# Kernel tuning notes

Hardware: AMD Instinct MI355X
Metric: run time of the kernel (lower is better)

The kernel has to match this reference:

```python
import jax, jax.numpy as jnp
import numpy as np
import math

D_MODEL = 1024
N_HEADS = 16
HEAD_DIM = D_MODEL // N_HEADS
PAD_INDEX = 0
NEG_INF = -1e9  # matches torch masked_fill value


def setup_inputs() -> dict:
    key = jax.random.key(0)
    ks = jax.random.split(key, 10)
    b, s = 2, 2048
    x = jax.random.normal(ks[0], (b, s, D_MODEL), dtype=jnp.float32)
    input_ids = jax.random.randint(ks[1], (b, s), 0, 32000, dtype=jnp.int64)
    scale = 1.0 / math.sqrt(D_MODEL)
    def lin(k):
        kw, kb = jax.random.split(k)
        W = jax.random.uniform(kw, (D_MODEL, D_MODEL), jnp.float32, -scale, scale)
        bb = jax.random.uniform(kb, (D_MODEL,), jnp.float32, -scale, scale)
        return W, bb
    Wq, bq = lin(ks[2])
    Wk, bk = lin(ks[3])
    Wv, bv = lin(ks[4])
    Wo, bo = lin(ks[5])
    return {"x": x, "input_ids": input_ids,
            "Wq": Wq, "bq": bq, "Wk": Wk, "bk": bk,
            "Wv": Wv, "bv": bv, "Wo": Wo, "bo": bo}


def reference(x, input_ids, Wq, bq, Wk, bk, Wv, bv, Wo, bo):
    b, s, _ = x.shape
    # torch nn.Linear: y = x @ W.T + b
    q = (x @ Wq.T + bq).reshape(b, s, N_HEADS, HEAD_DIM)
    k = (x @ Wk.T + bk).reshape(b, s, N_HEADS, HEAD_DIM)
    v = (x @ Wv.T + bv).reshape(b, s, N_HEADS, HEAD_DIM)
    # scores: [b, h, s, s]
    scores = jnp.einsum('bqhd,bkhd->bhqk', q, k) / math.sqrt(HEAD_DIM)
    pad_mask = (input_ids != PAD_INDEX)[:, None, None, :]          # [b,1,1,s] over keys
    causal = jnp.tril(jnp.ones((s, s), dtype=bool))[None, None]     # [1,1,s,s]
    final_mask = pad_mask & causal
    scores = jnp.where(final_mask, scores, NEG_INF)
    attn = jax.nn.softmax(scores, axis=-1)
    out = jnp.einsum('bhqk,bkhd->bqhd', attn, v).reshape(b, s, D_MODEL)
    return out @ Wo.T + bo
```

## Files before the change

### kernel.cpp

```cpp
#include <hip/hip_runtime.h>

#define DMODEL 1024
#define NHEADS 16
#define HDIM   64
#define BATCH  2
#define SEQ    2048
#define MROWS  (BATCH*SEQ)

typedef __bf16 bf16x8 __attribute__((ext_vector_type(8)));
typedef __bf16 bf16x4 __attribute__((ext_vector_type(4)));
typedef float floatx4 __attribute__((ext_vector_type(4)));

typedef const __attribute__((address_space(1))) void gvoid;
typedef __attribute__((address_space(3))) void lvoid;

template<bool V> struct ICb { static constexpr bool value = V; };

#define QSCALE 0.18033688011112042f

__global__ void cast_all(const float* __restrict__ x,
                         const float* __restrict__ wq, const float* __restrict__ wk,
                         const float* __restrict__ wv, const float* __restrict__ wo,
                         __bf16* __restrict__ xb, __bf16* __restrict__ wqb,
                         __bf16* __restrict__ wkb, __bf16* __restrict__ wvb,
                         __bf16* __restrict__ wob)
{
  const int i = blockIdx.x * 256 + threadIdx.x;
  const float* s; __bf16* o; int off;
  if (i < MROWS*DMODEL/4) { s = x; o = xb; off = i; }
  else {
    const int r = i - MROWS*DMODEL/4;
    const int w = r >> 18;
    off = r & 262143;
    s = (w == 0) ? wq : (w == 1) ? wk : (w == 2) ? wv : wo;
    o = (w == 0) ? wqb : (w == 1) ? wkb : (w == 2) ? wvb : wob;
  }
  const float4 f = ((const float4*)s)[off];
  bf16x4 v = {(__bf16)f.x, (__bf16)f.y, (__bf16)f.z, (__bf16)f.w};
  *(bf16x4*)(o + off*4) = v;
}

template<int MODE>
__global__ __launch_bounds__(256, 3)
void gemm_nt(const unsigned short* __restrict__ A,
             const unsigned short* __restrict__ W0,
             const unsigned short* __restrict__ W1,
             const unsigned short* __restrict__ W2,
             const float* __restrict__ b0,
             const float* __restrict__ b1,
             const float* __restrict__ b2,
             unsigned short* __restrict__ qout,
             unsigned short* __restrict__ kout,
             unsigned short* __restrict__ vout,
             float* __restrict__ outf)
{
  const int K = DMODEL;
  __shared__ unsigned short As[2][128*32];
  __shared__ unsigned short Bs[2][128*32];
  const int tid  = threadIdx.x;
  const int wid  = tid >> 6;
  const int lane = tid & 63;

  const int lin = blockIdx.x;
  const int wg  = (MODE == 0) ? ((lin & 7)*96 + (lin >> 3))
                              : ((lin & 7)*32 + (lin >> 3));
  const int bx  = (MODE == 0) ? (wg % 24) : (wg & 7);
  const int by  = (MODE == 0) ? (wg / 24) : (wg >> 3);
  const int brow = by * 128;
  const int bcol = bx * 128;
  const int wr = (wid >> 1) * 64;
  const int wc = (wid & 1) * 64;

  int which = 0;
  const unsigned short* Bw = W0;
  const float* bias = b0;
  int bcolL = bcol;
  if (MODE == 0) {
    which = bcol >> 10;
    Bw   = which == 0 ? W0 : which == 1 ? W1 : W2;
    bias = which == 0 ? b0 : which == 1 ? b1 : b2;
    bcolL = bcol & 1023;
  }

  floatx4 acc[4][4] = {};

  const int sr = wid*16 + (lane >> 2);
  const int sc = (lane & 3) * 8;
  const int fr = lane & 15;
  const int fk = (lane >> 4) * 8;

#define GSTAGE(KT, B) do {                                                     \
    _Pragma("unroll")                                                          \
    for (int i_ = 0; i_ < 2; ++i_) {                                           \
      __builtin_amdgcn_global_load_lds(                                        \
          (gvoid*)(A + (size_t)(brow + i_*64 + sr)*K + (KT) + sc),             \
          (lvoid*)(As[B] + i_*2048 + wid*512), 16, 0, 0);                      \
      __builtin_amdgcn_global_load_lds(                                        \
          (gvoid*)(Bw + (size_t)(bcolL + i_*64 + sr)*K + (KT) + sc),           \
          (lvoid*)(Bs[B] + i_*2048 + wid*512), 16, 0, 0);                      \
    }                                                                          \
  } while (0)

  GSTAGE(0, 0);

  for (int kt = 0; kt < K; kt += 32) {
    const int cur = (kt >> 5) & 1;
    if (kt + 32 < K) {
      GSTAGE(kt + 32, cur ^ 1);
      asm volatile("s_waitcnt vmcnt(4)" ::: "memory");
    } else {
      asm volatile("s_waitcnt vmcnt(0)" ::: "memory");
    }
    __builtin_amdgcn_s_barrier();
    __builtin_amdgcn_sched_barrier(0);

    bf16x8 af[4], bfv[4];
#pragma unroll
    for (int m = 0; m < 4; ++m)
      af[m] = *(const bf16x8*)(As[cur] + (wr + m*16 + fr)*32 + fk);
#pragma unroll
    for (int n = 0; n < 4; ++n)
      bfv[n] = *(const bf16x8*)(Bs[cur] + (wc + n*16 + fr)*32 + fk);
    __builtin_amdgcn_s_setprio(1);
#pragma unroll
    for (int m = 0; m < 4; ++m)
#pragma unroll
      for (int n = 0; n < 4; ++n)
        acc[m][n] = __builtin_amdgcn_mfma_f32_16x16x32_bf16(af[m], bfv[n], acc[m][n], 0, 0, 0);
    __builtin_amdgcn_s_setprio(0);
    __builtin_amdgcn_s_barrier();
  }
#undef GSTAGE

  const int er = (lane >> 4) * 4;
  const int ec = lane & 15;
#pragma unroll
  for (int m = 0; m < 4; ++m) {
#pragma unroll
    for (int n = 0; n < 4; ++n) {
      const int colL = bcolL + wc + n*16 + ec;
      const float bv = bias[colL];
      const int rowb = brow + wr + m*16 + er;
      if (MODE == 0) {
        const int bi = rowb >> 11, s = rowb & 2047;
        const int hh = colL >> 6, dd = colL & 63;
        if (which == 2) {
          bf16x4 v4 = {(__bf16)(acc[m][n][0] + bv), (__bf16)(acc[m][n][1] + bv),
                       (__bf16)(acc[m][n][2] + bv), (__bf16)(acc[m][n][3] + bv)};
          *(bf16x4*)((__bf16*)vout + ((size_t)(bi*NHEADS + hh)*HDIM + dd)*SEQ + s) = v4;
        } else if (which == 0) {
          __bf16* o = (__bf16*)qout;
#pragma unroll
          for (int j = 0; j < 4; ++j)
            o[((size_t)(bi*NHEADS + hh)*SEQ + s + j)*HDIM + dd] =
                (__bf16)((acc[m][n][j] + bv) * QSCALE);
        } else {
          __bf16* o = (__bf16*)kout;
#pragma unroll
          for (int j = 0; j < 4; ++j)
            o[((size_t)(bi*NHEADS + hh)*SEQ + s + j)*HDIM + dd] = (__bf16)(acc[m][n][j] + bv);
        }
      } else {
#pragma unroll
        for (int j = 0; j < 4; ++j)
          outf[(size_t)(rowb + j)*DMODEL + colL] = acc[m][n][j] + bv;
      }
    }
  }
}

__global__ __launch_bounds__(128, 4)
void attn_fwd(const unsigned short* __restrict__ qb,
              const unsigned short* __restrict__ kb,
              const unsigned short* __restrict__ vtb,
              const int* __restrict__ ids,
              unsigned short* __restrict__ outb)
{
  const int lin = blockIdx.x;
  const int k8 = lin >> 8;
  const int c8 = lin & 255;
  const int hb = c8 & 31;
  const int j  = c8 >> 5;
  const int qt = k8*8 + ((k8 & 1) ? 7 - j : j);
  const int h = hb & 15, bi = hb >> 4;

  const int tid = threadIdx.x, wid = tid >> 6, lane = tid & 63;
  const size_t hoff = (size_t)(bi*NHEADS + h) * SEQ * HDIM;
  const unsigned short* Qh  = qb  + hoff;
  const unsigned short* Kh  = kb  + hoff;
  const unsigned short* Vth = vtb + hoff;

  __shared__ unsigned short Ks[2][32*64];
  __shared__ unsigned short Vs[2][64*32];
  __shared__ unsigned short Ps[2][16*32];

  const int q_   = lane & 15;
  const int hi4  = lane >> 4;
  const int koff = hi4 * 4;
  const int qg = qt*32 + wid*16 + q_;

  bf16x8 qf[2];
#pragma unroll
  for (int c = 0; c < 2; ++c)
    qf[c] = *(const bf16x8*)(Qh + (size_t)qg*HDIM + c*32 + hi4*8);

  const int kr0 = tid >> 3;
  const int kc  = ((tid & 7) ^ (kr0 & 7)) * 8;
  const int vd0 = tid >> 2;
  const int vc  = ((tid & 3) ^ (vd0 & 3)) * 8;
  unsigned short* Pw = Ps[wid];

#define STAGE(T, B) do {                                                       \
    const unsigned short* kb_ = Kh + (size_t)(T)*32*HDIM;                      \
    const unsigned short* vb_ = Vth + (T)*32;                                  \
    __builtin_amdgcn_global_load_lds((gvoid*)(kb_ + kr0*HDIM + kc),            \
                                     (lvoid*)(Ks[B] + tid*8), 16, 0, 0);       \
    __builtin_amdgcn_global_load_lds((gvoid*)(kb_ + (kr0+16)*HDIM + kc),       \
                                     (lvoid*)(Ks[B] + (tid+128)*8), 16, 0, 0); \
    __builtin_amdgcn_global_load_lds((gvoid*)(vb_ + (size_t)vd0*SEQ + vc),     \
                                     (lvoid*)(Vs[B] + tid*8), 16, 0, 0);       \
    __builtin_amdgcn_global_load_lds((gvoid*)(vb_ + (size_t)(vd0+32)*SEQ + vc),\
                                     (lvoid*)(Vs[B] + (tid+128)*8), 16, 0, 0); \
  } while (0)

  float lsum = 0.f;
  floatx4 Oacc[4] = {};

  auto step = [&](auto Mc, int kb0, int bufc, unsigned int wm) {
    constexpr bool MASKED = decltype(Mc)::value;

    floatx4 st[2];
    __builtin_amdgcn_s_setprio(1);
#pragma unroll
    for (int t = 0; t < 2; ++t) {
      st[t] = (floatx4){0.f, 0.f, 0.f, 0.f};
      const int kr = t*16 + q_;
#pragma unroll
      for (int c = 0; c < 2; ++c) {
        bf16x8 kf = *(const bf16x8*)(Ks[bufc] + kr*64 + (((c*4 + hi4) ^ (q_ & 7)) * 8));
        st[t] = __builtin_amdgcn_mfma_f32_16x16x32_bf16(kf, qf[c], st[t], 0, 0, 0);
      }
    }
    __builtin_amdgcn_s_setprio(0);

    float ps = 0.f;
#pragma unroll
    for (int t = 0; t < 2; ++t) {
      float p[4];
#pragma unroll
      for (int r = 0; r < 4; ++r) {
        float pv = exp2f(st[t][r]);
        if (MASKED) {
          const int ko = t*16 + koff + r;
          const bool dead = ((kb0 + ko) > qg) || (((wm >> ko) & 1u) != 0u);
          pv = dead ? 0.f : pv;
        }
        p[r] = pv;
        ps += pv;
      }
      bf16x4 pk = {(__bf16)p[0], (__bf16)p[1], (__bf16)p[2], (__bf16)p[3]};
      const int ch = t*2 + (hi4 >> 1);
      *(bf16x4*)(Pw + q_*32 + ((ch ^ (q_ & 3)) * 8) + ((hi4 & 1) * 4)) = pk;
    }
    lsum += ps;

    bf16x8 pf = *(const bf16x8*)(Pw + q_*32 + ((hi4 ^ (q_ & 3)) * 8));
    __builtin_amdgcn_s_setprio(1);
#pragma unroll
    for (int n = 0; n < 4; ++n) {
      const int d = n*16 + q_;
      bf16x8 vf = *(const bf16x8*)(Vs[bufc] + d*32 + ((hi4 ^ (d & 3)) * 8));
      Oacc[n] = __builtin_amdgcn_mfma_f32_16x16x32_bf16(pf, vf, Oacc[n], 0, 0, 0);
    }
    __builtin_amdgcn_s_setprio(0);
  };

  const int nT = qt + 1;
  STAGE(0, 0);

  for (int kbv = 0; kbv < nT; ++kbv) {
    const int kb0 = kbv * 32;
    const int bufc = kbv & 1;
    const bool last = (kbv == nT - 1);
    const int pv = ids[bi*SEQ + kb0 + (lane & 31)];
    if (!last) {
      STAGE(kbv + 1, bufc ^ 1);
      asm volatile("s_waitcnt vmcnt(4)" ::: "memory");
    } else {
      asm volatile("s_waitcnt vmcnt(0)" ::: "memory");
    }
    const unsigned int wm = (unsigned int)__ballot(pv == 0);
    __builtin_amdgcn_s_barrier();
    __builtin_amdgcn_sched_barrier(0);

    if (!last && wm == 0u) step(ICb<false>{}, kb0, bufc, 0u);
    else                   step(ICb<true >{}, kb0, bufc, wm);
  }
#undef STAGE

  float lt = lsum + __shfl_xor(lsum, 16);
  lt += __shfl_xor(lt, 32);

#pragma unroll
  for (int r = 0; r < 4; ++r) {
    const float inv = 1.f / __shfl(lt, koff + r);
    const int row = bi*SEQ + qt*32 + wid*16 + koff + r;
#pragma unroll
    for (int n = 0; n < 4; ++n)
      ((__bf16*)outb)[(size_t)row*DMODEL + h*HDIM + n*16 + q_] = (__bf16)(Oacc[n][r] * inv);
  }
}

extern "C" void kernel_launch(void* const* d_in, const int* in_sizes, int n_in,
                              void* d_out, int out_size, void* d_ws, size_t ws_size,
                              hipStream_t stream)
{
  const float* x  = (const float*)d_in[0];
  const int*   ids= (const int*)d_in[1];
  const float* Wq = (const float*)d_in[2];
  const float* bq = (const float*)d_in[3];
  const float* Wk = (const float*)d_in[4];
  const float* bk = (const float*)d_in[5];
  const float* Wv = (const float*)d_in[6];
  const float* bv = (const float*)d_in[7];
  const float* Wo = (const float*)d_in[8];
  const float* bo = (const float*)d_in[9];
  float* out = (float*)d_out;

  char* ws = (char*)d_ws;
  unsigned short* xb   = (unsigned short*)(ws);
  unsigned short* wqb  = (unsigned short*)(ws + ( 8u<<20));
  unsigned short* wkb  = (unsigned short*)(ws + (10u<<20));
  unsigned short* wvb  = (unsigned short*)(ws + (12u<<20));
  unsigned short* wob  = (unsigned short*)(ws + (14u<<20));
  unsigned short* qbuf = (unsigned short*)(ws + (16u<<20));
  unsigned short* kbuf = (unsigned short*)(ws + (24u<<20));
  unsigned short* vbuf = (unsigned short*)(ws + (32u<<20));
  unsigned short* abuf = (unsigned short*)(ws + (40u<<20));

  cast_all<<<8192, 256, 0, stream>>>(x, Wq, Wk, Wv, Wo,
                                     (__bf16*)xb, (__bf16*)wqb, (__bf16*)wkb,
                                     (__bf16*)wvb, (__bf16*)wob);

  gemm_nt<0><<<768, 256, 0, stream>>>(xb, wqb, wkb, wvb, bq, bk, bv,
                                      qbuf, kbuf, vbuf, nullptr);

  attn_fwd<<<2048, 128, 0, stream>>>(qbuf, kbuf, vbuf, ids, abuf);

  gemm_nt<1><<<256, 256, 0, stream>>>(abuf, wob, wob, wob, bo, bo, bo,
                                      nullptr, nullptr, nullptr, out);
}
```

Baseline: 127.9 us.

## Enlarge attention tiles to 64 queries by 64 keys with four waves per block

The attention kernel now runs 256-thread blocks, each covering 64 query rows across four waves, and steps through keys in 64-wide tiles instead of 32. K/V tiles in shared memory double in size, and the pad mask ballot widens to 64 bits. The aim is to reuse each staged K/V tile across more queries and to halve the number of loop iterations and barriers. In exchange it uses more LDS per block, launches a 2D grid of 1024 blocks, adds a second barrier each iteration, and makes causal tiles coarser, so more masked work is computed on the diagonal.

```diff
diff --git a/kernel.cpp b/kernel.cpp
--- a/kernel.cpp
+++ b/kernel.cpp
@@ -169,75 +169,73 @@
   }
 }
 
-__global__ __launch_bounds__(128, 4)
+__global__ __launch_bounds__(256, 4)
 void attn_fwd(const unsigned short* __restrict__ qb,
               const unsigned short* __restrict__ kb,
               const unsigned short* __restrict__ vtb,
               const int* __restrict__ ids,
               unsigned short* __restrict__ outb)
 {
-  const int lin = blockIdx.x;
-  const int k8 = lin >> 8;
-  const int c8 = lin & 255;
-  const int hb = c8 & 31;
-  const int j  = c8 >> 5;
-  const int qt = k8*8 + ((k8 & 1) ? 7 - j : j);
+  const int hb = blockIdx.x;
   const int h = hb & 15, bi = hb >> 4;
+  const int y = blockIdx.y;
+  const int jm = y >> 3, mm = y & 7;
+  const int qt = jm*8 + ((jm & 1) ? 7 - mm : mm);
 
   const int tid = threadIdx.x, wid = tid >> 6, lane = tid & 63;
+  const int qbase = qt * 64;
   const size_t hoff = (size_t)(bi*NHEADS + h) * SEQ * HDIM;
   const unsigned short* Qh  = qb  + hoff;
   const unsigned short* Kh  = kb  + hoff;
   const unsigned short* Vth = vtb + hoff;
 
-  __shared__ unsigned short Ks[2][32*64];
-  __shared__ unsigned short Vs[2][64*32];
-  __shared__ unsigned short Ps[2][16*32];
+  __shared__ unsigned short Ks[2][64*64];
+  __shared__ unsigned short Vs[2][64*64];
+  __shared__ unsigned short Ps[4][16*64];
 
   const int q_   = lane & 15;
   const int hi4  = lane >> 4;
   const int koff = hi4 * 4;
-  const int qg = qt*32 + wid*16 + q_;
+  const int qg = qbase + wid*16 + q_;
 
   bf16x8 qf[2];
 #pragma unroll
   for (int c = 0; c < 2; ++c)
     qf[c] = *(const bf16x8*)(Qh + (size_t)qg*HDIM + c*32 + hi4*8);
 
-  const int kr0 = tid >> 3;
-  const int kc  = ((tid & 7) ^ (kr0 & 7)) * 8;
-  const int vd0 = tid >> 2;
-  const int vc  = ((tid & 3) ^ (vd0 & 3)) * 8;
+  const int r0 = tid >> 3;
+  const int sw = ((tid & 7) ^ (r0 & 7)) * 8;
   unsigned short* Pw = Ps[wid];
 
 #define STAGE(T, B) do {                                                       \
-    const unsigned short* kb_ = Kh + (size_t)(T)*32*HDIM;                      \
-    const unsigned short* vb_ = Vth + (T)*32;                                  \
-    __builtin_amdgcn_global_load_lds((gvoid*)(kb_ + kr0*HDIM + kc),            \
+    const unsigned short* kbase_ = Kh + (size_t)((T)*64) * HDIM;               \
+    const unsigned short* vbase_ = Vth + (T)*64;                               \
+    __builtin_amdgcn_global_load_lds((gvoid*)(kbase_ + r0*64 + sw),            \
                                      (lvoid*)(Ks[B] + tid*8), 16, 0, 0);       \
-    __builtin_amdgcn_global_load_lds((gvoid*)(kb_ + (kr0+16)*HDIM + kc),       \
-                                     (lvoid*)(Ks[B] + (tid+128)*8), 16, 0, 0); \
-    __builtin_amdgcn_global_load_lds((gvoid*)(vb_ + (size_t)vd0*SEQ + vc),     \
+    __builtin_amdgcn_global_load_lds((gvoid*)(kbase_ + (r0+32)*64 + sw),       \
+                                     (lvoid*)(Ks[B] + (tid+256)*8), 16, 0, 0); \
+    __builtin_amdgcn_global_load_lds((gvoid*)(vbase_ + (size_t)r0*SEQ + sw),   \
                                      (lvoid*)(Vs[B] + tid*8), 16, 0, 0);       \
-    __builtin_amdgcn_global_load_lds((gvoid*)(vb_ + (size_t)(vd0+32)*SEQ + vc),\
-                                     (lvoid*)(Vs[B] + (tid+128)*8), 16, 0, 0); \
+    __builtin_amdgcn_global_load_lds((gvoid*)(vbase_ + (size_t)(r0+32)*SEQ + sw),\
+                                     (lvoid*)(Vs[B] + (tid+256)*8), 16, 0, 0); \
   } while (0)
 
   float lsum = 0.f;
   floatx4 Oacc[4] = {};
 
-  auto step = [&](auto Mc, int kb0, int bufc, unsigned int wm) {
+  auto step = [&](auto Mc, int kb0, int bufc, unsigned long long wm) {
     constexpr bool MASKED = decltype(Mc)::value;
 
-    floatx4 st[2];
+    floatx4 st[4];
     __builtin_amdgcn_s_setprio(1);
 #pragma unroll
-    for (int t = 0; t < 2; ++t) {
+    for (int t = 0; t < 4; ++t) {
       st[t] = (floatx4){0.f, 0.f, 0.f, 0.f};
       const int kr = t*16 + q_;
 #pragma unroll
       for (int c = 0; c < 2; ++c) {
-        bf16x8 kf = *(const bf16x8*)(Ks[bufc] + kr*64 + (((c*4 + hi4) ^ (q_ & 7)) * 8));
+        const int cd = ((c*4 + hi4) ^ (kr & 7)) * 8;
+        bf16x8 kf = *(const bf16x8*)(Ks[bufc] + kr*64 + cd);
         st[t] = __builtin_amdgcn_mfma_f32_16x16x32_bf16(kf, qf[c], st[t], 0, 0, 0);
       }
     }
@@ -245,32 +243,37 @@
 
     float ps = 0.f;
 #pragma unroll
-    for (int t = 0; t < 2; ++t) {
+    for (int t = 0; t < 4; ++t) {
       float p[4];
 #pragma unroll
       for (int r = 0; r < 4; ++r) {
         float pv = exp2f(st[t][r]);
         if (MASKED) {
           const int ko = t*16 + koff + r;
-          const bool dead = ((kb0 + ko) > qg) || (((wm >> ko) & 1u) != 0u);
+          const bool dead = ((kb0 + ko) > qg) || (((wm >> ko) & 1ull) != 0ull);
           pv = dead ? 0.f : pv;
         }
         p[r] = pv;
         ps += pv;
       }
       bf16x4 pk = {(__bf16)p[0], (__bf16)p[1], (__bf16)p[2], (__bf16)p[3]};
-      const int ch = t*2 + (hi4 >> 1);
-      *(bf16x4*)(Pw + q_*32 + ((ch ^ (q_ & 3)) * 8) + ((hi4 & 1) * 4)) = pk;
+      const int ko = t*16 + koff;
+      *(bf16x4*)(Pw + q_*64 + (((ko >> 3) ^ (q_ & 7)) * 8) + (ko & 7)) = pk;
     }
     lsum += ps;
 
-    bf16x8 pf = *(const bf16x8*)(Pw + q_*32 + ((hi4 ^ (q_ & 3)) * 8));
     __builtin_amdgcn_s_setprio(1);
 #pragma unroll
-    for (int n = 0; n < 4; ++n) {
-      const int d = n*16 + q_;
-      bf16x8 vf = *(const bf16x8*)(Vs[bufc] + d*32 + ((hi4 ^ (d & 3)) * 8));
-      Oacc[n] = __builtin_amdgcn_mfma_f32_16x16x32_bf16(pf, vf, Oacc[n], 0, 0, 0);
+    for (int cp = 0; cp < 2; ++cp) {
+      const int ko = cp*32 + hi4*8;
+      bf16x8 pf = *(const bf16x8*)(Pw + q_*64 + (((ko >> 3) ^ (q_ & 7)) * 8));
+#pragma unroll
+      for (int n = 0; n < 4; ++n) {
+        const int d = n*16 + q_;
+        const int cd = ((cp*4 + hi4) ^ (d & 7)) * 8;
+        bf16x8 vf = *(const bf16x8*)(Vs[bufc] + d*64 + cd);
+        Oacc[n] = __builtin_amdgcn_mfma_f32_16x16x32_bf16(pf, vf, Oacc[n], 0, 0, 0);
+      }
     }
     __builtin_amdgcn_s_setprio(0);
   };
@@ -279,22 +282,23 @@
   STAGE(0, 0);
 
   for (int kbv = 0; kbv < nT; ++kbv) {
-    const int kb0 = kbv * 32;
+    const int kb0 = kbv * 64;
     const int bufc = kbv & 1;
     const bool last = (kbv == nT - 1);
-    const int pv = ids[bi*SEQ + kb0 + (lane & 31)];
+    const int pv = ids[bi*SEQ + kb0 + lane];
     if (!last) {
       STAGE(kbv + 1, bufc ^ 1);
       asm volatile("s_waitcnt vmcnt(4)" ::: "memory");
     } else {
       asm volatile("s_waitcnt vmcnt(0)" ::: "memory");
     }
-    const unsigned int wm = (unsigned int)__ballot(pv == 0);
+    const unsigned long long wm = __ballot(pv == 0);
     __builtin_amdgcn_s_barrier();
     __builtin_amdgcn_sched_barrier(0);
 
-    if (!last && wm == 0u) step(ICb<false>{}, kb0, bufc, 0u);
-    else                   step(ICb<true >{}, kb0, bufc, wm);
+    if (!last && wm == 0ull) step(ICb<false>{}, kb0, bufc, 0ull);
+    else                     step(ICb<true >{}, kb0, bufc, wm);
+    __builtin_amdgcn_s_barrier();
   }
 #undef STAGE
 
@@ -304,7 +308,7 @@
 #pragma unroll
   for (int r = 0; r < 4; ++r) {
     const float inv = 1.f / __shfl(lt, koff + r);
-    const int row = bi*SEQ + qt*32 + wid*16 + koff + r;
+    const int row = bi*SEQ + qbase + wid*16 + koff + r;
 #pragma unroll
     for (int n = 0; n < 4; ++n)
       ((__bf16*)outb)[(size_t)row*DMODEL + h*HDIM + n*16 + q_] = (__bf16)(Oacc[n][r] * inv);
@@ -345,7 +349,7 @@
   gemm_nt<0><<<768, 256, 0, stream>>>(xb, wqb, wkb, wvb, bq, bk, bv,
                                       qbuf, kbuf, vbuf, nullptr);
 
-  attn_fwd<<<2048, 128, 0, stream>>>(qbuf, kbuf, vbuf, ids, abuf);
+  attn_fwd<<<dim3(32, 32), 256, 0, stream>>>(qbuf, kbuf, vbuf, ids, abuf);
 
   gemm_nt<1><<<256, 256, 0, stream>>>(abuf, wob, wob, wob, bo, bo, bo,
                                       nullptr, nullptr, nullptr, out);
```

After: 116.8 us. 8.6% less time.
